# Optimization experiments

Measured on AMD Instinct MI355X. Metric: run time of the kernel, lower is better.

## Reference

```python
import jax, jax.numpy as jnp
import numpy as np

# Model dims (ViT-Base @ 384)
L, H, D, HD, M, P, IMG, B, NC, CH = 12, 12, 768, 64, 3072, 16, 384, 32, 1000, 3
NPATCH = (IMG // P) ** 2  # 576
SCALE = 1.0 / np.sqrt(HD)


def setup_inputs() -> dict:
    key = jax.random.key(0)
    ks = iter(jax.random.split(key, 16))
    def n(shape, s=0.02):
        return (jax.random.normal(next(ks), shape, jnp.float32) * s).astype(jnp.float32)
    return dict(
        x=jax.random.normal(next(ks), (B, CH, IMG, IMG), jnp.float32),
        conv_w=n((D, CH, P, P)), conv_b=jnp.zeros((D,), jnp.float32),
        cls_token=jnp.zeros((1, 1, D), jnp.float32),
        pos_emb=n((1, NPATCH + 1, D), 1.0),
        ln1_g=jnp.ones((L, D), jnp.float32), ln1_b=jnp.zeros((L, D), jnp.float32),
        wqkv=n((L, H, D, 3 * HD)), bqkv=jnp.zeros((L, H, 3 * HD), jnp.float32),
        wmsa=n((L, D, D)), bmsa=jnp.zeros((L, D), jnp.float32),
        ln2_g=jnp.ones((L, D), jnp.float32), ln2_b=jnp.zeros((L, D), jnp.float32),
        lnm_g=jnp.ones((L, D), jnp.float32), lnm_b=jnp.zeros((L, D), jnp.float32),
        w1=n((L, D, M)), b1=jnp.zeros((L, M), jnp.float32),
        w2=n((L, M, D)), b2=jnp.zeros((L, D), jnp.float32),
        lnf_g=jnp.ones((D,), jnp.float32), lnf_b=jnp.zeros((D,), jnp.float32),
        whead=n((D, NC)), bhead=jnp.zeros((NC,), jnp.float32),
    )


def _ln(x, g, b, eps=1e-5):
    mu = jnp.mean(x, axis=-1, keepdims=True)
    var = jnp.mean(jnp.square(x - mu), axis=-1, keepdims=True)
    return (x - mu) * jax.lax.rsqrt(var + eps) * g + b


def _encoder_block(x, p):
    (ln1_g, ln1_b, wqkv, bqkv, wmsa, bmsa,
     ln2_g, ln2_b, lnm_g, lnm_b, w1, b1, w2, b2) = p
    b = x.shape[0]
    h = _ln(x, ln1_g, ln1_b)
    # batched per-head QKV (math identical to looping over H small Linears)
    qkv = jnp.einsum('bsd,hde->bhse', h, wqkv) + bqkv[:, None, :]  # [B,H,S,3*HD]
    q, k, v = jnp.split(qkv, 3, axis=-1)
    attn = jax.nn.softmax(jnp.einsum('bhqe,bhke->bhqk', q, k) * SCALE, axis=-1)
    o = jnp.einsum('bhqk,bhke->bhqe', attn, v)          # [B,H,S,HD]
    o = o.transpose(0, 2, 1, 3).reshape(b, -1, D)        # concat heads along feature
    msa = jnp.einsum('bsd,de->bse', o, wmsa) + bmsa
    x1 = h + msa                                          # residual around MSA (post-LN1)
    h2 = _ln(x1, ln2_g, ln2_b)
    h2 = _ln(h2, lnm_g, lnm_b)                            # MLPBlock's own LayerNorm (double LN, faithful)
    mlp = jnp.einsum('bsm,md->bsd', jax.nn.gelu(jnp.einsum('bsd,dm->bsm', h2, w1) + b1, approximate=False), w2) + b2
    return x1 + mlp, None


def reference(x, conv_w, conv_b, cls_token, pos_emb,
              ln1_g, ln1_b, wqkv, bqkv, wmsa, bmsa,
              ln2_g, ln2_b, lnm_g, lnm_b, w1, b1, w2, b2,
              lnf_g, lnf_b, whead, bhead):
    b = x.shape[0]
    # patchify conv (image divisible by patch, so F.pad is a no-op)
    t = jax.lax.conv_general_dilated(x, conv_w, (P, P), 'VALID',
                                     dimension_numbers=('NCHW', 'OIHW', 'NCHW'))
    t = t + conv_b[None, :, None, None]
    # faithful to torch .view(b, -1, embed_dim) on NCHW layout (channel-major flatten)
    t = t.reshape(b, -1, D)
    n = t.shape[1]
    t = jnp.concatenate([jnp.broadcast_to(cls_token, (b, 1, D)), t], axis=1)
    t = t + pos_emb[:, :n + 1]
    stacked = (ln1_g, ln1_b, wqkv, bqkv, wmsa, bmsa,
               ln2_g, ln2_b, lnm_g, lnm_b, w1, b1, w2, b2)
    t, _ = jax.lax.scan(_encoder_block, t, stacked)
    y = _ln(t[:, 0], lnf_g, lnf_b)
    y = jax.nn.softmax(jnp.einsum('bd,dc->bc', y, whead) + bhead, axis=-1)
    return y
```

## Files before the change

kernel.cpp:

```cpp
#include <hip/hip_runtime.h>

using f16   = _Float16;
using f16x8 = __attribute__((ext_vector_type(8))) _Float16;
using f32x4 = __attribute__((ext_vector_type(4))) float;

#define MPAD  18560
#define MREAL 18464
#define MCONV 18432
#define SEQ   577
#define SPAD  640
#define NHEAD 12
#define NBATCH 32
#define SCALE_ 0.125f

__device__ __forceinline__ void load_lds16(const void* g, void* l) {
  __builtin_amdgcn_global_load_lds(
      (const __attribute__((address_space(1))) void*)g,
      (__attribute__((address_space(3))) void*)l, 16, 0, 0);
}

template<int K, int EPI>
__global__ __launch_bounds__(256) void gemm_k(
    const f16* __restrict__ A, const f16* __restrict__ Bt,
    const float* __restrict__ bias, const float* __restrict__ res,
    float* __restrict__ o32, f16* __restrict__ o16a, f16* __restrict__ o16b,
    f16* __restrict__ o16c, const float* __restrict__ pos, int N, int Mreal)
{
  __shared__ __align__(16) f16 As[128*32];
  __shared__ __align__(16) f16 Bs[128*32];
  const int tid = threadIdx.x;
  const int lane = tid & 63, wv = tid >> 6;

  const int gx = gridDim.x, gy = gridDim.y;
  const int nwg = gx * gy;
  const int flat = blockIdx.y * gx + blockIdx.x;
  const int xcd = flat & 7;
  const int qq = nwg >> 3, rr = nwg & 7;
  const int p_ = ((xcd < rr) ? xcd * (qq + 1) : rr * (qq + 1) + (xcd - rr) * qq)
                 + (flat >> 3);
  const int bandsz = gy * 6;
  const int band = p_ / bandsz, within = p_ - band * bandsz;
  const int byi = within / 6;
  const int bxi = band * 6 + (within - byi * 6);
  const int bm = byi << 7, bn = bxi << 7;

  const int wm = (wv >> 1) << 6, wn = (wv & 1) << 6;
  const int r16 = lane & 15, g4 = lane >> 4;
  const f32x4 Z4 = {0.f, 0.f, 0.f, 0.f};

  f32x4 acc[4][4];
#pragma unroll
  for (int m = 0; m < 4; ++m)
#pragma unroll
    for (int n = 0; n < 4; ++n) acc[m][n] = Z4;

  const int soff = wv * 1024 + lane * 8;
  for (int k0 = 0; k0 < K; k0 += 32) {
#pragma unroll
    for (int j = 0; j < 2; ++j) {
      int off = soff + j * 512;
      int row = off >> 5;
      int cs  = (off >> 3) & 3;
      int gc  = cs ^ (row & 3);
      load_lds16(A  + (size_t)(bm + row) * K + k0 + gc * 8, As + (wv*2 + j) * 512);
      load_lds16(Bt + (size_t)(bn + row) * K + k0 + gc * 8, Bs + (wv*2 + j) * 512);
    }
    __syncthreads();
    f16x8 af[4], bf[4];
#pragma unroll
    for (int m = 0; m < 4; ++m) {
      int row = wm + m * 16 + r16;
      af[m] = *(const f16x8*)(As + row * 32 + ((g4 ^ (row & 3)) << 3));
    }
#pragma unroll
    for (int n = 0; n < 4; ++n) {
      int row = wn + n * 16 + r16;
      bf[n] = *(const f16x8*)(Bs + row * 32 + ((g4 ^ (row & 3)) << 3));
    }
#pragma unroll
    for (int m = 0; m < 4; ++m)
#pragma unroll
      for (int n = 0; n < 4; ++n)
        acc[m][n] = __builtin_amdgcn_mfma_f32_16x16x32_f16(af[m], bf[n], acc[m][n], 0, 0, 0);
    __syncthreads();
  }

#pragma unroll
  for (int m = 0; m < 4; ++m) {
#pragma unroll
    for (int n = 0; n < 4; ++n) {
#pragma unroll
      for (int r = 0; r < 4; ++r) {
        int grow = bm + wm + m * 16 + g4 * 4 + r;
        int gcol = bn + wn + n * 16 + r16;
        float v = acc[m][n][r];
        if constexpr (EPI == 0) {
          if (grow < Mreal) {
            int b = grow / 576, p = grow - b * 576;
            int i = gcol * 576 + p;
            int sp = i / 768, dd = i - sp * 768;
            o32[((size_t)(b * SEQ + sp + 1)) * 768 + dd] =
                v + bias[gcol] + pos[(size_t)(sp + 1) * 768 + dd];
          }
        } else if constexpr (EPI == 1) {
          if (grow < Mreal) {
            int b = grow / SEQ, s = grow - b * SEQ;
            int hq = gcol / 192, rem = gcol - hq * 192;
            int sel = rem >> 6, e = rem & 63;
            float val = v + bias[gcol];
            int bh = b * NHEAD + hq;
            if (sel == 0)      o16a[((size_t)bh * SPAD + s) * 64 + e] = (f16)val;
            else if (sel == 1) o16b[((size_t)bh * SPAD + s) * 64 + e] = (f16)val;
            else               o16c[((size_t)bh * 64 + e) * SPAD + s] = (f16)val;
          }
        } else if constexpr (EPI == 2) {
          size_t idx = (size_t)grow * N + gcol;
          o32[idx] = v + bias[gcol] + res[idx];
        } else {
          float val = v + bias[gcol];
          float gl = 0.5f * val * (1.0f + erff(val * 0.70710678f));
          o16a[(size_t)grow * N + gcol] = (f16)gl;
        }
      }
    }
  }
}

__device__ __forceinline__ void block_red2(float& a, float& b, float* sm, int tid) {
  __syncthreads();
#pragma unroll
  for (int d = 32; d; d >>= 1) { a += __shfl_down(a, d); b += __shfl_down(b, d); }
  if ((tid & 63) == 0) { int w = tid >> 6; sm[w] = a; sm[w + 4] = b; }
  __syncthreads();
  a = sm[0] + sm[1] + sm[2] + sm[3];
  b = sm[4] + sm[5] + sm[6] + sm[7];
}

__global__ __launch_bounds__(256) void ln_fwd(const float* __restrict__ X,
    const float* __restrict__ g, const float* __restrict__ bb,
    float* __restrict__ ho, f16* __restrict__ hh)
{
  int row = blockIdx.x, tid = threadIdx.x;
  const float* x = X + (size_t)row * 768;
  float v0 = x[tid], v1 = x[tid + 256], v2 = x[tid + 512];
  float s = v0 + v1 + v2, s2 = v0*v0 + v1*v1 + v2*v2;
  __shared__ float sm[8];
  block_red2(s, s2, sm, tid);
  float mu = s * (1.f/768.f);
  float var = s2 * (1.f/768.f) - mu * mu;
  float rs = rsqrtf(var + 1e-5f);
  size_t base = (size_t)row * 768;
  float y0 = (v0 - mu) * rs * g[tid      ] + bb[tid      ];
  float y1 = (v1 - mu) * rs * g[tid + 256] + bb[tid + 256];
  float y2 = (v2 - mu) * rs * g[tid + 512] + bb[tid + 512];
  ho[base + tid] = y0; ho[base + tid + 256] = y1; ho[base + tid + 512] = y2;
  hh[base + tid] = (f16)y0; hh[base + tid + 256] = (f16)y1; hh[base + tid + 512] = (f16)y2;
}

__global__ __launch_bounds__(256) void ln2_fwd(const float* __restrict__ X,
    const float* __restrict__ g2, const float* __restrict__ bb2,
    const float* __restrict__ gm, const float* __restrict__ bbm,
    f16* __restrict__ hh)
{
  int row = blockIdx.x, tid = threadIdx.x;
  const float* x = X + (size_t)row * 768;
  float v0 = x[tid], v1 = x[tid + 256], v2 = x[tid + 512];
  float s = v0 + v1 + v2, s2 = v0*v0 + v1*v1 + v2*v2;
  __shared__ float sm[8];
  block_red2(s, s2, sm, tid);
  float mu = s * (1.f/768.f), var = s2 * (1.f/768.f) - mu * mu;
  float rs = rsqrtf(var + 1e-5f);
  float y0 = (v0 - mu) * rs * g2[tid      ] + bb2[tid      ];
  float y1 = (v1 - mu) * rs * g2[tid + 256] + bb2[tid + 256];
  float y2 = (v2 - mu) * rs * g2[tid + 512] + bb2[tid + 512];
  s = y0 + y1 + y2; s2 = y0*y0 + y1*y1 + y2*y2;
  block_red2(s, s2, sm, tid);
  mu = s * (1.f/768.f); var = s2 * (1.f/768.f) - mu * mu;
  rs = rsqrtf(var + 1e-5f);
  size_t base = (size_t)row * 768;
  hh[base + tid      ] = (f16)((y0 - mu) * rs * gm[tid      ] + bbm[tid      ]);
  hh[base + tid + 256] = (f16)((y1 - mu) * rs * gm[tid + 256] + bbm[tid + 256]);
  hh[base + tid + 512] = (f16)((y2 - mu) * rs * gm[tid + 512] + bbm[tid + 512]);
}

__global__ __launch_bounds__(256) void attn_k(const f16* __restrict__ qbuf,
    const f16* __restrict__ kbuf, const f16* __restrict__ vtbuf,
    f16* __restrict__ obuf)
{
  const int bh = blockIdx.y;
  const int b = bh / NHEAD, hd = bh - b * NHEAD;
  const int s0 = blockIdx.x << 6;
  const int tid = threadIdx.x, lane = tid & 63, wv = tid >> 6;
  const int r16 = lane & 15, g4 = lane >> 4;
  const f16* Q  = qbuf  + (size_t)bh * SPAD * 64;
  const f16* Kg = kbuf  + (size_t)bh * SPAD * 64;
  const f16* Vg = vtbuf + (size_t)bh * 64 * SPAD;
  __shared__ __align__(16) f16 Kt[64 * 64];
  __shared__ __align__(16) f16 Vt[64 * 64];
  __shared__ __align__(16) f16 Pw[4][16][72];
  const f32x4 Z4 = {0.f, 0.f, 0.f, 0.f};

  f16x8 qf[2];
  {
    const f16* qr = Q + (size_t)(s0 + wv * 16 + r16) * 64;
    qf[0] = *(const f16x8*)(qr + g4 * 8);
    qf[1] = *(const f16x8*)(qr + 32 + g4 * 8);
  }
  float m_run[4] = {-1e30f, -1e30f, -1e30f, -1e30f};
  float l_run[4] = {0.f, 0.f, 0.f, 0.f};
  f32x4 o_acc[4];
#pragma unroll
  for (int n = 0; n < 4; ++n) o_acc[n] = Z4;

  for (int kt = 0; kt < SPAD; kt += 64) {
#pragma unroll
    for (int j = 0; j < 2; ++j) {
      int off = (wv * 2 + j) * 1024 + lane * 16;
      int row = off >> 7;
      int cs  = (off >> 4) & 7;
      int gc  = cs ^ (row & 7);
      load_lds16(Kg + (size_t)(kt + row) * 64 + gc * 8, (void*)((char*)Kt + (wv*2 + j) * 1024));
      load_lds16(Vg + (size_t)row * SPAD + kt + gc * 8, (void*)((char*)Vt + (wv*2 + j) * 1024));
    }
    __syncthreads();

    f32x4 sa[4];
#pragma unroll
    for (int n = 0; n < 4; ++n) sa[n] = Z4;
#pragma unroll
    for (int n = 0; n < 4; ++n) {
      int krow = n * 16 + r16;
#pragma unroll
      for (int kc = 0; kc < 2; ++kc) {
        f16x8 kf = *(const f16x8*)(Kt + krow * 64 + (((kc * 4 + g4) ^ (krow & 7)) << 3));
        sa[n] = __builtin_amdgcn_mfma_f32_16x16x32_f16(qf[kc], kf, sa[n], 0, 0, 0);
      }
    }
#pragma unroll
    for (int r = 0; r < 4; ++r) {
      float mx = -1e30f;
#pragma unroll
      for (int n = 0; n < 4; ++n) {
        int key = kt + n * 16 + r16;
        float sv = (key < SEQ) ? sa[n][r] * SCALE_ : -1e30f;
        sa[n][r] = sv;
        mx = fmaxf(mx, sv);
      }
#pragma unroll
      for (int d = 1; d < 16; d <<= 1) mx = fmaxf(mx, __shfl_xor(mx, d));
      float mnew = fmaxf(m_run[r], mx);
      float alpha = __expf(m_run[r] - mnew);
      m_run[r] = mnew;
      float ssum = 0.f;
#pragma unroll
      for (int n = 0; n < 4; ++n) {
        float p = __expf(sa[n][r] - mnew);
        ssum += p;
        Pw[wv][g4 * 4 + r][n * 16 + r16] = (f16)p;
      }
#pragma unroll
      for (int d = 1; d < 16; d <<= 1) ssum += __shfl_xor(ssum, d);
      l_run[r] = l_run[r] * alpha + ssum;
#pragma unroll
      for (int n = 0; n < 4; ++n) o_acc[n][r] *= alpha;
    }
    f16x8 pf[2];
    pf[0] = *(const f16x8*)(&Pw[wv][r16][g4 * 8]);
    pf[1] = *(const f16x8*)(&Pw[wv][r16][32 + g4 * 8]);
#pragma unroll
    for (int n = 0; n < 4; ++n) {
      int erow = n * 16 + r16;
#pragma unroll
      for (int kc = 0; kc < 2; ++kc) {
        f16x8 vf = *(const f16x8*)(Vt + erow * 64 + (((kc * 4 + g4) ^ (erow & 7)) << 3));
        o_acc[n] = __builtin_amdgcn_mfma_f32_16x16x32_f16(pf[kc], vf, o_acc[n], 0, 0, 0);
      }
    }
    __syncthreads();
  }
  float inv[4];
#pragma unroll
  for (int r = 0; r < 4; ++r) inv[r] = 1.f / l_run[r];
#pragma unroll
  for (int n = 0; n < 4; ++n)
#pragma unroll
    for (int r = 0; r < 4; ++r) {
      int s = s0 + wv * 16 + g4 * 4 + r;
      if (s < SEQ)
        obuf[((size_t)(b * SEQ + s)) * 768 + hd * 64 + n * 16 + r16] =
            (f16)(o_acc[n][r] * inv[r]);
    }
}

__global__ __launch_bounds__(256) void cvt_transpose(const float* __restrict__ in,
    f16* __restrict__ out, int K, int N, size_t ls_in, size_t ls_out)
{
  in  += (size_t)blockIdx.z * ls_in;
  out += (size_t)blockIdx.z * ls_out;
  __shared__ float t[32][33];
  int n0 = blockIdx.x << 5, k0 = blockIdx.y << 5;
  int tx = threadIdx.x & 31, ty = threadIdx.x >> 5;
#pragma unroll
  for (int i = 0; i < 4; ++i) t[ty + 8*i][tx] = in[(size_t)(k0 + ty + 8*i) * N + n0 + tx];
  __syncthreads();
#pragma unroll
  for (int i = 0; i < 4; ++i) out[(size_t)(n0 + ty + 8*i) * K + k0 + tx] = (f16)t[tx][ty + 8*i];
}

__global__ __launch_bounds__(256) void cvt_qkvw(const float* __restrict__ in,
    f16* __restrict__ out, size_t ls_in, size_t ls_out)
{
  in  += (size_t)blockIdx.z * ls_in;
  out += (size_t)blockIdx.z * ls_out;
  __shared__ float t[32][33];
  int n0 = blockIdx.x << 5, k0 = blockIdx.y << 5;
  int tx = threadIdx.x & 31, ty = threadIdx.x >> 5;
  int hq = n0 / 192, r0 = n0 - hq * 192;
#pragma unroll
  for (int i = 0; i < 4; ++i)
    t[ty + 8*i][tx] = in[(size_t)hq * 147456 + (size_t)(k0 + ty + 8*i) * 192 + r0 + tx];
  __syncthreads();
#pragma unroll
  for (int i = 0; i < 4; ++i) out[(size_t)(n0 + ty + 8*i) * 768 + k0 + tx] = (f16)t[tx][ty + 8*i];
}

__global__ __launch_bounds__(256) void cvt_plain(const float* __restrict__ in,
    f16* __restrict__ out, int n)
{
  int i = blockIdx.x * 1024 + threadIdx.x;
#pragma unroll
  for (int j = 0; j < 4; ++j) { int idx = i + j * 256; if (idx < n) out[idx] = (f16)in[idx]; }
}

__global__ __launch_bounds__(256) void zero_vpad(f16* __restrict__ vtb) {
  int bh = blockIdx.x;
  for (int idx = threadIdx.x; idx < 64 * (SPAD - SEQ); idx += 256) {
    int e = idx / (SPAD - SEQ), s = SEQ + idx - e * (SPAD - SEQ);
    vtb[((size_t)bh * 64 + e) * SPAD + s] = (f16)0.f;
  }
}

__global__ __launch_bounds__(256) void im2col_k(const float* __restrict__ x, f16* __restrict__ out) {
  int row = blockIdx.x;
  int b = row / 576, p = row - b * 576;
  int py = p / 24, px = p - py * 24;
  int tid = threadIdx.x;
#pragma unroll
  for (int j = 0; j < 3; ++j) {
    int k = tid + j * 256;
    int c = k >> 8, rem = k & 255;
    int iy = rem >> 4, ix = rem & 15;
    out[(size_t)row * 768 + k] =
        (f16)x[(((size_t)(b * 3 + c)) * 384 + py * 16 + iy) * 384 + px * 16 + ix];
  }
}

__global__ __launch_bounds__(256) void cls_k(const float* __restrict__ ct,
    const float* __restrict__ pos, float* __restrict__ X)
{
  int b = blockIdx.x, tid = threadIdx.x;
#pragma unroll
  for (int j = 0; j < 3; ++j) {
    int d0 = tid + j * 256;
    X[((size_t)b * SEQ) * 768 + d0] = ct[d0] + pos[d0];
  }
}

__global__ __launch_bounds__(256) void head_k(const float* __restrict__ X,
    const float* __restrict__ g, const float* __restrict__ bb,
    const float* __restrict__ W, const float* __restrict__ bhd,
    float* __restrict__ out)
{
  int b = blockIdx.x, tid = threadIdx.x;
  const float* x = X + (size_t)(b * SEQ) * 768;
  float v0 = x[tid], v1 = x[tid + 256], v2 = x[tid + 512];
  float s = v0 + v1 + v2, s2 = v0*v0 + v1*v1 + v2*v2;
  __shared__ float sm[8];
  block_red2(s, s2, sm, tid);
  float mu = s * (1.f/768.f), var = s2 * (1.f/768.f) - mu * mu;
  float rs = rsqrtf(var + 1e-5f);
  __shared__ float y[768];
  y[tid      ] = (v0 - mu) * rs * g[tid      ] + bb[tid      ];
  y[tid + 256] = (v1 - mu) * rs * g[tid + 256] + bb[tid + 256];
  y[tid + 512] = (v2 - mu) * rs * g[tid + 512] + bb[tid + 512];
  __syncthreads();
  float lg[4];
#pragma unroll
  for (int j = 0; j < 4; ++j) {
    int c = tid + j * 256;
    float acc = (c < 1000) ? bhd[c] : -1e30f;
    if (c < 1000)
      for (int d = 0; d < 768; ++d) acc = fmaf(y[d], W[(size_t)d * 1000 + c], acc);
    lg[j] = acc;
  }
  float mx = fmaxf(fmaxf(lg[0], lg[1]), fmaxf(lg[2], lg[3]));
#pragma unroll
  for (int d = 32; d; d >>= 1) mx = fmaxf(mx, __shfl_down(mx, d));
  if ((tid & 63) == 0) sm[tid >> 6] = mx;
  __syncthreads();
  mx = fmaxf(fmaxf(sm[0], sm[1]), fmaxf(sm[2], sm[3]));
  float ex[4], se = 0.f;
#pragma unroll
  for (int j = 0; j < 4; ++j) {
    int c = tid + j * 256;
    ex[j] = (c < 1000) ? __expf(lg[j] - mx) : 0.f;
    se += ex[j];
  }
  __syncthreads();
#pragma unroll
  for (int d = 32; d; d >>= 1) se += __shfl_down(se, d);
  if ((tid & 63) == 0) sm[tid >> 6] = se;
  __syncthreads();
  se = sm[0] + sm[1] + sm[2] + sm[3];
  float inv = 1.f / se;
#pragma unroll
  for (int j = 0; j < 4; ++j) {
    int c = tid + j * 256;
    if (c < 1000) out[(size_t)b * 1000 + c] = ex[j] * inv;
  }
}

extern "C" void kernel_launch(void* const* d_in, const int* in_sizes, int n_in,
                              void* d_out, int out_size, void* d_ws, size_t ws_size,
                              hipStream_t stream)
{
  (void)in_sizes; (void)n_in; (void)out_size;
  const float* x      = (const float*)d_in[0];
  const float* conv_w = (const float*)d_in[1];
  const float* conv_b = (const float*)d_in[2];
  const float* cls_t  = (const float*)d_in[3];
  const float* pos    = (const float*)d_in[4];
  const float* ln1_g  = (const float*)d_in[5];
  const float* ln1_b  = (const float*)d_in[6];
  const float* wqkv   = (const float*)d_in[7];
  const float* bqkv   = (const float*)d_in[8];
  const float* wmsa   = (const float*)d_in[9];
  const float* bmsa   = (const float*)d_in[10];
  const float* ln2_g  = (const float*)d_in[11];
  const float* ln2_b  = (const float*)d_in[12];
  const float* lnm_g  = (const float*)d_in[13];
  const float* lnm_b  = (const float*)d_in[14];
  const float* w1     = (const float*)d_in[15];
  const float* b1     = (const float*)d_in[16];
  const float* w2     = (const float*)d_in[17];
  const float* b2     = (const float*)d_in[18];
  const float* lnf_g  = (const float*)d_in[19];
  const float* lnf_b  = (const float*)d_in[20];
  const float* whead  = (const float*)d_in[21];
  const float* bhead  = (const float*)d_in[22];
  float* out = (float*)d_out;

  const size_t szQ  = (size_t)2304 * 768;
  const size_t szM  = (size_t)768 * 768;
  const size_t szW1 = (size_t)3072 * 768;
  const size_t szW2 = (size_t)768 * 3072;
  const size_t fixed_bytes =
      (size_t)MPAD * 768 * 4 + (size_t)MPAD * 768 * 4 + (size_t)MPAD * 768 * 2 +
      (size_t)MPAD * 3072 * 2 + 3 * ((size_t)NBATCH * NHEAD * SPAD * 64 * 2) +
      (size_t)768 * 768 * 2  + 16 * 256 ;
  const bool hoist =
      ws_size >= fixed_bytes + 12 * (szQ + szM + szW1 + szW2) * 2 + 8 * 256;
  const int LW = hoist ? 12 : 1;

  char* wsp = (char*)d_ws;
  size_t off = 0;
  auto alloc = [&](size_t bytes) {
    char* p = wsp + off; off += (bytes + 255) & ~(size_t)255; return p;
  };
  float* X    = (float*)alloc((size_t)MPAD * 768 * 4);
  float* hbf  = (float*)alloc((size_t)MPAD * 768 * 4);
  f16*   hh   = (f16*)  alloc((size_t)MPAD * 768 * 2);
  f16*   abuf = (f16*)  alloc((size_t)MPAD * 3072 * 2);
  f16*   qb   = (f16*)  alloc((size_t)NBATCH * NHEAD * SPAD * 64 * 2);
  f16*   kb   = (f16*)  alloc((size_t)NBATCH * NHEAD * SPAD * 64 * 2);
  f16*   vtb  = (f16*)  alloc((size_t)NBATCH * NHEAD * SPAD * 64 * 2);
  f16*   WcT  = (f16*)  alloc((size_t)768 * 768 * 2);
  f16*   WqkvT= (f16*)  alloc(LW * szQ  * 2);
  f16*   WmsaT= (f16*)  alloc(LW * szM  * 2);
  f16*   W1T  = (f16*)  alloc(LW * szW1 * 2);
  f16*   W2T  = (f16*)  alloc(LW * szW2 * 2);
  f16*   obuf   = abuf;
  f16*   patchA = abuf;
  f16*   h2h    = hh;
  if (ws_size < off) return;

  zero_vpad<<<dim3(NBATCH * NHEAD), 256, 0, stream>>>(vtb);
  cvt_plain<<<dim3((768 * 768 + 1023) / 1024), 256, 0, stream>>>(conv_w, WcT, 768 * 768);
  if (hoist) {
    cvt_qkvw<<<dim3(72, 24, 12), 256, 0, stream>>>(wqkv, WqkvT, (size_t)12*768*192, szQ);
    cvt_transpose<<<dim3(24, 24, 12), 256, 0, stream>>>(wmsa, WmsaT, 768, 768, szM, szM);
    cvt_transpose<<<dim3(96, 24, 12), 256, 0, stream>>>(w1, W1T, 768, 3072, szW1, szW1);
    cvt_transpose<<<dim3(24, 96, 12), 256, 0, stream>>>(w2, W2T, 3072, 768, szW2, szW2);
  }
  im2col_k<<<dim3(MCONV), 256, 0, stream>>>(x, patchA);
  gemm_k<768, 0><<<dim3(6, 144), 256, 0, stream>>>(
      patchA, WcT, conv_b, nullptr, X, nullptr, nullptr, nullptr, pos, 768, MCONV);
  cls_k<<<dim3(NBATCH), 256, 0, stream>>>(cls_t, pos, X);

  for (int l = 0; l < 12; ++l) {
    f16* wq  = WqkvT + (hoist ? (size_t)l * szQ  : 0);
    f16* wms = WmsaT + (hoist ? (size_t)l * szM  : 0);
    f16* w1t = W1T   + (hoist ? (size_t)l * szW1 : 0);
    f16* w2t = W2T   + (hoist ? (size_t)l * szW2 : 0);
    if (!hoist) {
      cvt_qkvw<<<dim3(72, 24), 256, 0, stream>>>(
          wqkv + (size_t)l * 12 * 768 * 192, wq, 0, 0);
      cvt_transpose<<<dim3(24, 24), 256, 0, stream>>>(
          wmsa + (size_t)l * 768 * 768, wms, 768, 768, 0, 0);
      cvt_transpose<<<dim3(96, 24), 256, 0, stream>>>(
          w1 + (size_t)l * 768 * 3072, w1t, 768, 3072, 0, 0);
      cvt_transpose<<<dim3(24, 96), 256, 0, stream>>>(
          w2 + (size_t)l * 3072 * 768, w2t, 3072, 768, 0, 0);
    }

    ln_fwd<<<dim3(MREAL), 256, 0, stream>>>(X, ln1_g + l * 768, ln1_b + l * 768, hbf, hh);
    gemm_k<768, 1><<<dim3(18, 145), 256, 0, stream>>>(
        hh, wq, bqkv + (size_t)l * 2304, nullptr, nullptr, qb, kb, vtb, nullptr, 2304, MREAL);
    attn_k<<<dim3(10, NBATCH * NHEAD), 256, 0, stream>>>(qb, kb, vtb, obuf);
    gemm_k<768, 2><<<dim3(6, 145), 256, 0, stream>>>(
        obuf, wms, bmsa + l * 768, hbf, X, nullptr, nullptr, nullptr, nullptr, 768, MREAL);
    ln2_fwd<<<dim3(MREAL), 256, 0, stream>>>(
        X, ln2_g + l * 768, ln2_b + l * 768, lnm_g + l * 768, lnm_b + l * 768, h2h);
    gemm_k<768, 3><<<dim3(24, 145), 256, 0, stream>>>(
        h2h, w1t, b1 + (size_t)l * 3072, nullptr, nullptr, abuf, nullptr, nullptr, nullptr, 3072, MREAL);
    gemm_k<3072, 2><<<dim3(6, 145), 256, 0, stream>>>(
        abuf, w2t, b2 + l * 768, X, X, nullptr, nullptr, nullptr, nullptr, 768, MREAL);
  }
  head_k<<<dim3(NBATCH), 256, 0, stream>>>(X, lnf_g, lnf_b, whead, bhead, out);
}
```

Baseline: 8.300 ms.

## Triple-buffer GEMM LDS staging and split classifier head into parallel kernels

The GEMM main loop now uses three LDS buffers and prefetches tile t+2 while computing tile t. Explicit vmcnt waits and one barrier per iteration replace the load-then-sync pattern, so global-to-LDS latency overlaps with MFMA work. The head is split into a logits kernel spread over 4x more blocks with 4-way accumulators, followed by a separate softmax kernel. This raises LDS use to 48KB per block, which may reduce occupancy, and the hand-written waitcnt logic relies on the count of outstanding loads being exactly right.

```diff
diff --git a/kernel.cpp b/kernel.cpp
--- a/kernel.cpp
+++ b/kernel.cpp
@@ -26,8 +26,10 @@
     float* __restrict__ o32, f16* __restrict__ o16a, f16* __restrict__ o16b,
     f16* __restrict__ o16c, const float* __restrict__ pos, int N, int Mreal)
 {
-  __shared__ __align__(16) f16 As[128*32];
-  __shared__ __align__(16) f16 Bs[128*32];
+  static_assert(K % 32 == 0, "BK=32");
+  constexpr int NT = K / 32;
+  __shared__ __align__(16) f16 As[3][128 * 32];
+  __shared__ __align__(16) f16 Bs[3][128 * 32];
   const int tid = threadIdx.x;
   const int lane = tid & 63, wv = tid >> 6;
 
@@ -55,34 +57,51 @@
     for (int n = 0; n < 4; ++n) acc[m][n] = Z4;
 
   const int soff = wv * 1024 + lane * 8;
-  for (int k0 = 0; k0 < K; k0 += 32) {
-#pragma unroll
-    for (int j = 0; j < 2; ++j) {
-      int off = soff + j * 512;
-      int row = off >> 5;
-      int cs  = (off >> 3) & 3;
-      int gc  = cs ^ (row & 3);
-      load_lds16(A  + (size_t)(bm + row) * K + k0 + gc * 8, As + (wv*2 + j) * 512);
-      load_lds16(Bt + (size_t)(bn + row) * K + k0 + gc * 8, Bs + (wv*2 + j) * 512);
-    }
-    __syncthreads();
+  const int r0   = soff >> 5;
+  const int gc0  = ((soff >> 3) & 3) ^ (r0 & 3);
+  const f16* Agp = A  + (size_t)(bm + r0) * K + gc0 * 8;
+  const f16* Bgp = Bt + (size_t)(bn + r0) * K + gc0 * 8;
+  const int ldso = wv * 1024;
+
+  auto stage = [&](f16* Ad, f16* Bd, int k0) {
+    load_lds16(Agp + k0,                  Ad + ldso);
+    load_lds16(Agp + (size_t)16 * K + k0, Ad + ldso + 512);
+    load_lds16(Bgp + k0,                  Bd + ldso);
+    load_lds16(Bgp + (size_t)16 * K + k0, Bd + ldso + 512);
+  };
+
+  f16 *A0 = As[0], *A1 = As[1], *A2 = As[2];
+  f16 *B0 = Bs[0], *B1 = Bs[1], *B2 = Bs[2];
+  stage(A0, B0, 0);
+  stage(A1, B1, 32);
+  asm volatile("s_waitcnt vmcnt(4)" ::: "memory");
+  __builtin_amdgcn_s_barrier();
+
+#pragma unroll 1
+  for (int t = 0; t < NT; ++t) {
+    const bool pf = (t + 2 < NT);
+    if (pf) stage(A2, B2, (t + 2) * 32);
     f16x8 af[4], bf[4];
 #pragma unroll
     for (int m = 0; m < 4; ++m) {
       int row = wm + m * 16 + r16;
-      af[m] = *(const f16x8*)(As + row * 32 + ((g4 ^ (row & 3)) << 3));
+      af[m] = *(const f16x8*)(A0 + row * 32 + ((g4 ^ (row & 3)) << 3));
     }
 #pragma unroll
     for (int n = 0; n < 4; ++n) {
       int row = wn + n * 16 + r16;
-      bf[n] = *(const f16x8*)(Bs + row * 32 + ((g4 ^ (row & 3)) << 3));
+      bf[n] = *(const f16x8*)(B0 + row * 32 + ((g4 ^ (row & 3)) << 3));
     }
 #pragma unroll
     for (int m = 0; m < 4; ++m)
 #pragma unroll
       for (int n = 0; n < 4; ++n)
         acc[m][n] = __builtin_amdgcn_mfma_f32_16x16x32_f16(af[m], bf[n], acc[m][n], 0, 0, 0);
-    __syncthreads();
+    if (pf) { asm volatile("s_waitcnt vmcnt(4)" ::: "memory"); }
+    else    { asm volatile("s_waitcnt vmcnt(0)" ::: "memory"); }
+    __builtin_amdgcn_s_barrier();
+    f16* ta = A0; A0 = A1; A1 = A2; A2 = ta;
+    f16* tb = B0; B0 = B1; B1 = B2; B2 = tb;
   }
 
 #pragma unroll
@@ -366,10 +385,10 @@
   }
 }
 
-__global__ __launch_bounds__(256) void head_k(const float* __restrict__ X,
+__global__ __launch_bounds__(256) void head_logits(const float* __restrict__ X,
     const float* __restrict__ g, const float* __restrict__ bb,
     const float* __restrict__ W, const float* __restrict__ bhd,
-    float* __restrict__ out)
+    float* __restrict__ lg)
 {
   int b = blockIdx.x, tid = threadIdx.x;
   const float* x = X + (size_t)(b * SEQ) * 768;
@@ -384,26 +403,42 @@
   y[tid + 256] = (v1 - mu) * rs * g[tid + 256] + bb[tid + 256];
   y[tid + 512] = (v2 - mu) * rs * g[tid + 512] + bb[tid + 512];
   __syncthreads();
-  float lg[4];
+  int c = blockIdx.y * 250 + tid;
+  if (tid < 250) {
+    float a0 = 0.f, a1 = 0.f, a2 = 0.f, a3 = 0.f;
+#pragma unroll 4
+    for (int d = 0; d < 768; d += 4) {
+      a0 = fmaf(y[d    ], W[(size_t)(d    ) * 1000 + c], a0);
+      a1 = fmaf(y[d + 1], W[(size_t)(d + 1) * 1000 + c], a1);
+      a2 = fmaf(y[d + 2], W[(size_t)(d + 2) * 1000 + c], a2);
+      a3 = fmaf(y[d + 3], W[(size_t)(d + 3) * 1000 + c], a3);
+    }
+    lg[(size_t)b * 1000 + c] = (a0 + a1) + (a2 + a3) + bhd[c];
+  }
+}
+
+__global__ __launch_bounds__(256) void head_soft(const float* __restrict__ lg,
+    float* __restrict__ out)
+{
+  int b = blockIdx.x, tid = threadIdx.x;
+  __shared__ float sm[8];
+  float v[4], mx = -1e30f;
 #pragma unroll
   for (int j = 0; j < 4; ++j) {
     int c = tid + j * 256;
-    float acc = (c < 1000) ? bhd[c] : -1e30f;
-    if (c < 1000)
-      for (int d = 0; d < 768; ++d) acc = fmaf(y[d], W[(size_t)d * 1000 + c], acc);
-    lg[j] = acc;
-  }
-  float mx = fmaxf(fmaxf(lg[0], lg[1]), fmaxf(lg[2], lg[3]));
+    v[j] = (c < 1000) ? lg[(size_t)b * 1000 + c] : -1e30f;
+    mx = fmaxf(mx, v[j]);
+  }
 #pragma unroll
   for (int d = 32; d; d >>= 1) mx = fmaxf(mx, __shfl_down(mx, d));
   if ((tid & 63) == 0) sm[tid >> 6] = mx;
   __syncthreads();
   mx = fmaxf(fmaxf(sm[0], sm[1]), fmaxf(sm[2], sm[3]));
-  float ex[4], se = 0.f;
+  float se = 0.f, ex[4];
 #pragma unroll
   for (int j = 0; j < 4; ++j) {
     int c = tid + j * 256;
-    ex[j] = (c < 1000) ? __expf(lg[j] - mx) : 0.f;
+    ex[j] = (c < 1000) ? __expf(v[j] - mx) : 0.f;
     se += ex[j];
   }
   __syncthreads();
@@ -482,6 +517,7 @@
   f16*   obuf   = abuf;
   f16*   patchA = abuf;
   f16*   h2h    = hh;
+  float* lgbuf  = hbf;
   if (ws_size < off) return;
 
   zero_vpad<<<dim3(NBATCH * NHEAD), 256, 0, stream>>>(vtb);
@@ -526,5 +562,6 @@
     gemm_k<3072, 2><<<dim3(6, 145), 256, 0, stream>>>(
         abuf, w2t, b2 + l * 768, X, X, nullptr, nullptr, nullptr, nullptr, 768, MREAL);
   }
-  head_k<<<dim3(NBATCH), 256, 0, stream>>>(X, lnf_g, lnf_b, whead, bhead, out);
-}
+  head_logits<<<dim3(NBATCH, 4), 256, 0, stream>>>(X, lnf_g, lnf_b, whead, bhead, lgbuf);
+  head_soft<<<dim3(NBATCH), 256, 0, stream>>>(lgbuf, out);
+}
```

New measurement: 8.463 ms. Within noise of the previous version (+2.0%).
